# Kernel tuning notes

Hardware: AMD Instinct MI355X
Metric: run time of the kernel (lower is better)

## Reference

```python
import jax, jax.numpy as jnp
import numpy as np

DIM = 512
D_IN = 4096
N_OBJ = 2048
N_REL = 32768
STEPS = 2
N_OBJ_CLS = 151
N_REL_CLS = 51
EPS = 1e-5


def _mlp2(x, w1, b1, w2, b2):
    # Linear -> ReLU -> Linear (torch Linear: y = x W^T + b)
    return jnp.maximum(x @ w1.T + b1, 0.0) @ w2.T + b2


def _gate(a, b, w, bias):
    # Sequential(Linear(2*dim, 1), Sigmoid) on cat([a, b], 1)
    return jax.nn.sigmoid(jnp.concatenate([a, b], axis=1) @ w.T + bias)


def _gru_cell(x, h, wih, whh, bih, bhh):
    gi = x @ wih.T + bih  # [N, 3*DIM]
    gh = h @ whh.T + bhh
    ir, iz, inew = jnp.split(gi, 3, axis=1)
    hr, hz, hnew = jnp.split(gh, 3, axis=1)
    r = jax.nn.sigmoid(ir + hr)
    z = jax.nn.sigmoid(iz + hz)
    n = jnp.tanh(inew + r * hnew)
    return (1.0 - z) * n + z * h


def setup_inputs() -> dict:
    key = jax.random.key(0)
    ks = jax.random.split(key, 32)
    rn = lambda k, shape, s=0.02: jax.random.normal(k, shape, dtype=jnp.float32) * s
    z = lambda *shape: jnp.zeros(shape, dtype=jnp.float32)
    return {
        'x_obj': jax.random.normal(ks[0], (N_OBJ, D_IN), dtype=jnp.float32),
        'x_pred': jax.random.normal(ks[1], (N_REL, D_IN), dtype=jnp.float32),
        'rel_inds': jax.random.randint(ks[2], (N_REL, 2), 0, N_OBJ),
        # obj / pred embedding MLPs
        'oe_w1': rn(ks[3], (DIM, D_IN)), 'oe_b1': z(DIM),
        'oe_w2': rn(ks[4], (DIM, DIM)), 'oe_b2': z(DIM),
        'pe_w1': rn(ks[5], (DIM, D_IN)), 'pe_b1': z(DIM),
        'pe_w2': rn(ks[6], (DIM, DIM)), 'pe_b2': z(DIM),
        # gates: Linear(2*dim, 1)
        'g_sn_w': rn(ks[7], (1, 2 * DIM)), 'g_sn_b': z(1),
        'g_on_w': rn(ks[8], (1, 2 * DIM)), 'g_on_b': z(1),
        'g_se_w': rn(ks[9], (1, 2 * DIM)), 'g_se_b': z(1),
        'g_oe_w': rn(ks[10], (1, 2 * DIM)), 'g_oe_b': z(1),
        # GRU cells
        'ngru_wih': rn(ks[11], (3 * DIM, DIM)), 'ngru_whh': rn(ks[12], (3 * DIM, DIM)),
        'ngru_bih': z(3 * DIM), 'ngru_bhh': z(3 * DIM),
        'egru_wih': rn(ks[13], (3 * DIM, DIM)), 'egru_whh': rn(ks[14], (3 * DIM, DIM)),
        'egru_bih': z(3 * DIM), 'egru_bhh': z(3 * DIM),
        # classifier heads
        'op_w': rn(ks[15], (N_OBJ_CLS, DIM)), 'op_b': z(N_OBJ_CLS),
        'pp_w': rn(ks[16], (N_REL_CLS, DIM)), 'pp_b': z(N_REL_CLS),
    }


def reference(x_obj, x_pred, rel_inds,
              oe_w1, oe_b1, oe_w2, oe_b2,
              pe_w1, pe_b1, pe_w2, pe_b2,
              g_sn_w, g_sn_b, g_on_w, g_on_b,
              g_se_w, g_se_b, g_oe_w, g_oe_b,
              ngru_wih, ngru_whh, ngru_bih, ngru_bhh,
              egru_wih, egru_whh, egru_bih, egru_bhh,
              op_w, op_b, pp_w, pp_b):
    n_obj = x_obj.shape[0]
    subj_idx = rel_inds[:, 0]
    obj_idx = rel_inds[:, 1]

    h_obj = _mlp2(x_obj, oe_w1, oe_b1, oe_w2, oe_b2)    # [N_obj, DIM]
    h_edge = _mlp2(x_pred, pe_w1, pe_b1, pe_w2, pe_b2)  # [N_rel, DIM]

    # row sums of the 0/1 subj/obj_pred_map == in-degree counts (constants)
    ones = jnp.ones((rel_inds.shape[0],), dtype=jnp.float32)
    cnt_s = jax.ops.segment_sum(ones, subj_idx, num_segments=n_obj)[:, None]
    cnt_o = jax.ops.segment_sum(ones, obj_idx, num_segments=n_obj)[:, None]

    for _ in range(STEPS):
        sub_vert = h_obj[subj_idx]  # [N_rel, DIM]
        obj_vert = h_obj[obj_idx]

        # node update: gated edge->node messages, mean-aggregated per node
        msg_p2s = _gate(sub_vert, h_edge, g_sn_w, g_sn_b) * h_edge
        msg_p2o = _gate(obj_vert, h_edge, g_on_w, g_on_b) * h_edge
        node_message = (
            jax.ops.segment_sum(msg_p2s, subj_idx, num_segments=n_obj) / (cnt_s + EPS)
            + jax.ops.segment_sum(msg_p2o, obj_idx, num_segments=n_obj) / (cnt_o + EPS)
        ) / 2.0
        new_h_obj = _gru_cell(node_message, h_obj, ngru_wih, ngru_whh, ngru_bih, ngru_bhh)

        # edge update: gated node->edge messages
        msg_s2p = _gate(sub_vert, h_edge, g_se_w, g_se_b) * sub_vert
        msg_o2p = _gate(obj_vert, h_edge, g_oe_w, g_oe_b) * obj_vert
        edge_message = (msg_s2p + msg_o2p) / 2.0
        h_edge = _gru_cell(edge_message, h_edge, egru_wih, egru_whh, egru_bih, egru_bhh)
        h_obj = new_h_obj

    obj_class_logits = h_obj @ op_w.T + op_b    # [N_obj, 151]
    pred_class_logits = h_edge @ pp_w.T + pp_b  # [N_rel, 51]
    obj_class_labels = jnp.argmax(obj_class_logits[:, 1:], axis=1) + 1
    return (h_obj, h_edge, obj_class_logits, pred_class_logits, obj_class_labels, rel_inds)
```

## Files before the change

kernel.cpp:

```cpp
#include <hip/hip_runtime.h>
#include <math.h>

typedef unsigned short u16;
typedef unsigned int u32;
typedef _Float16 f16;
typedef f16 f16x8 __attribute__((ext_vector_type(8)));
typedef float f32x4 __attribute__((ext_vector_type(4)));

#define DIM 512
#define D_IN 4096
#define N_OBJS 2048
#define N_RELS 32768
#define N_OBJ_CLS 151
#define N_REL_CLS 51
#define EPSV 1e-5f

#define OFF_HOBJ  0
#define OFF_HEDGE (N_OBJS*DIM)
#define OFF_OLOG  (OFF_HEDGE + N_RELS*DIM)
#define OFF_PLOG  (OFF_OLOG + N_OBJS*N_OBJ_CLS)
#define OFF_LBL   (OFF_PLOG + N_RELS*N_REL_CLS)
#define OFF_RI    (OFF_LBL + N_OBJS)

__device__ __forceinline__ float sigmoidf_(float x) { return 1.0f / (1.0f + expf(-x)); }
__device__ __forceinline__ u16 f2h_(float f) {
    union { f16 h; u16 u; } c; c.h = (f16)f; return c.u;
}
__device__ __forceinline__ float h2f_(u16 u) {
    union { f16 h; u16 u; } c; c.u = u; return (float)c.h;
}

__device__ __forceinline__ void cvt8h1(const float* f, uint4& h) {
    u32 hh[8];
#pragma unroll
    for (int i = 0; i < 8; i++) hh[i] = f2h_(f[i]);
    h.x = hh[0] | (hh[1] << 16); h.y = hh[2] | (hh[3] << 16);
    h.z = hh[4] | (hh[5] << 16); h.w = hh[6] | (hh[7] << 16);
}
__device__ __forceinline__ void cvt8h2(const float* f, uint4& h, uint4& l) {
    u32 hh[8], ll[8];
#pragma unroll
    for (int i = 0; i < 8; i++) {
        u16 x = f2h_(f[i]);
        hh[i] = x;
        ll[i] = f2h_(f[i] - h2f_(x));
    }
    h.x = hh[0] | (hh[1] << 16); h.y = hh[2] | (hh[3] << 16);
    h.z = hh[4] | (hh[5] << 16); h.w = hh[6] | (hh[7] << 16);
    l.x = ll[0] | (ll[1] << 16); l.y = ll[2] | (ll[3] << 16);
    l.z = ll[4] | (ll[5] << 16); l.w = ll[6] | (ll[7] << 16);
}

__device__ __forceinline__ int swzo(int row, int c) {
    return row * 32 + ((c ^ ((row >> 1) & 3)) << 3);
}

__device__ __forceinline__ int xcdswz(int orig, int nwg) {
    const int q = nwg >> 3;
    return (orig & 7) * q + (orig >> 3);
}

__device__ __forceinline__ void gload16(const void* g, void* l) {
    __builtin_amdgcn_global_load_lds(
        (const __attribute__((address_space(1))) void*)g,
        (__attribute__((address_space(3))) void*)l, 16, 0, 0);
}

__global__ __launch_bounds__(256) void convert_h(const float* __restrict__ src,
    u16* __restrict__ hi, int n4)
{
    const int i = blockIdx.x * 256 + threadIdx.x;
    if (i >= n4) return;
    const float4 v = ((const float4*)src)[i];
    ((ushort4*)hi)[i] = make_ushort4(f2h_(v.x), f2h_(v.y), f2h_(v.z), f2h_(v.w));
}

template<bool RELU, int AT, bool WSPLIT>
__global__ __launch_bounds__(256, 3) void gemm_a32(
    const float* __restrict__ A, const u16* __restrict__ Bhi,
    const float* __restrict__ bias, u16* __restrict__ Chi, u16* __restrict__ Clo,
    int NX, int K)
{
    __shared__ u16 sAh[128 * 32], sBh[128 * 32];
    __shared__ u16 sAl[AT == 2 ? 128 * 32 : 1];
    const int id = xcdswz(blockIdx.x, gridDim.x);
    const int m0 = (id / NX) * 128, n0 = (id % NX) * 128;
    const int N = NX * 128;
    const int t = threadIdx.x;
    const int wid = t >> 6, lane = t & 63;
    const int wm = (wid >> 1) * 64, wn = (wid & 1) * 64;
    const int lr = lane & 15, lk = lane >> 4;

    f32x4 acc[4][4] = {};

    const int sr = t >> 1;
    const int sc = (t & 1) * 2;
    const float* Ap = A + (size_t)(m0 + sr) * K + (t & 1) * 16;

    const int rB = (wid * 2) * 16 + (lane >> 2);
    const int cB = (lane & 3) ^ ((rB >> 1) & 3);
    const u16* Bp0 = Bhi + (size_t)(n0 + rB) * K + cB * 8;
    const u16* Bp1 = Bp0 + (size_t)16 * K;
    u16* Bd0 = &sBh[(wid * 2) * 512];
    u16* Bd1 = Bd0 + 512;

    float fv[16];
    *(float4*)&fv[0]  = *(const float4*)(Ap);
    *(float4*)&fv[4]  = *(const float4*)(Ap + 4);
    *(float4*)&fv[8]  = *(const float4*)(Ap + 8);
    *(float4*)&fv[12] = *(const float4*)(Ap + 12);

    for (int k0 = 0; k0 < K; k0 += 32) {
        uint4 ah0, ah1, al0, al1;
        if (AT == 2) { cvt8h2(fv, ah0, al0); cvt8h2(fv + 8, ah1, al1); }
        else         { cvt8h1(fv, ah0);      cvt8h1(fv + 8, ah1); }

        __syncthreads();
        gload16(Bp0 + k0, Bd0);
        gload16(Bp1 + k0, Bd1);
        *(uint4*)&sAh[swzo(sr, sc)]     = ah0;
        *(uint4*)&sAh[swzo(sr, sc + 1)] = ah1;
        if (AT == 2) {
            *(uint4*)&sAl[swzo(sr, sc)]     = al0;
            *(uint4*)&sAl[swzo(sr, sc + 1)] = al1;
        }
        asm volatile("s_waitcnt vmcnt(0)" ::: "memory");
        __syncthreads();

        const int kn = k0 + 32;
        if (kn < K) {
            *(float4*)&fv[0]  = *(const float4*)(Ap + kn);
            *(float4*)&fv[4]  = *(const float4*)(Ap + kn + 4);
            *(float4*)&fv[8]  = *(const float4*)(Ap + kn + 8);
            *(float4*)&fv[12] = *(const float4*)(Ap + kn + 12);
        }

        f16x8 ah[4], al[4], bh[4];
#pragma unroll
        for (int f = 0; f < 4; f++) {
            const int off = swzo(wm + f * 16 + lr, lk);
            ah[f] = *(const f16x8*)&sAh[off];
            if (AT == 2) al[f] = *(const f16x8*)&sAl[off];
            bh[f] = *(const f16x8*)&sBh[swzo(wn + f * 16 + lr, lk)];
        }
#pragma unroll
        for (int fm = 0; fm < 4; fm++)
#pragma unroll
            for (int fn = 0; fn < 4; fn++) {
                acc[fm][fn] = __builtin_amdgcn_mfma_f32_16x16x32_f16(ah[fm], bh[fn], acc[fm][fn], 0, 0, 0);
                if (AT == 2)
                    acc[fm][fn] = __builtin_amdgcn_mfma_f32_16x16x32_f16(al[fm], bh[fn], acc[fm][fn], 0, 0, 0);
            }
    }
#pragma unroll
    for (int fm = 0; fm < 4; fm++) {
        const int mrow = m0 + wm + fm * 16 + lk * 4;
#pragma unroll
        for (int fn = 0; fn < 4; fn++) {
            const int col = n0 + wn + fn * 16 + lr;
            const float bv = bias[col];
#pragma unroll
            for (int j = 0; j < 4; j++) {
                float v = acc[fm][fn][j] + bv;
                if (RELU) v = fmaxf(v, 0.0f);
                const u16 h = f2h_(v);
                Chi[(size_t)(mrow + j) * N + col] = h;
                if (WSPLIT) Clo[(size_t)(mrow + j) * N + col] = f2h_(v - h2f_(h));
            }
        }
    }
}

template<int AT, bool WF32, bool WHI, bool WLO>
__global__ __launch_bounds__(256, AT == 1 ? 4 : 3) void gemm_f16(
    const u16* __restrict__ Ahi, const u16* __restrict__ Alo,
    const u16* __restrict__ Bhi, const float* __restrict__ bias,
    float* __restrict__ C32, u16* __restrict__ Chi, u16* __restrict__ Clo,
    int NX, int N, int ldc, int K)
{
    __shared__ u16 sAh[128 * 32], sBh[128 * 32];
    __shared__ u16 sAl[AT == 2 ? 128 * 32 : 1];
    const int id = xcdswz(blockIdx.x, gridDim.x);
    const int m0 = (id / NX) * 128, n0 = (id % NX) * 128;
    const int t = threadIdx.x;
    const int wid = t >> 6, lane = t & 63;
    const int wm = (wid >> 1) * 64, wn = (wid & 1) * 64;
    const int lr = lane & 15, lk = lane >> 4;

    f32x4 acc[4][4] = {};

    const int rr = (wid * 2) * 16 + (lane >> 2);
    const int cc = (lane & 3) ^ ((rr >> 1) & 3);
    const u16* pA0 = Ahi + (size_t)(m0 + rr) * K + cc * 8;
    const u16* pA1 = pA0 + (size_t)16 * K;
    const u16* pL0 = (AT == 2) ? Alo + (size_t)(m0 + rr) * K + cc * 8 : nullptr;
    const u16* pL1 = (AT == 2) ? pL0 + (size_t)16 * K : nullptr;
    const u16* pB0 = Bhi + (size_t)(n0 + rr) * K + cc * 8;
    const u16* pB1 = pB0 + (size_t)16 * K;
    u16* dA0 = &sAh[(wid * 2) * 512]; u16* dA1 = dA0 + 512;
    u16* dL0 = &sAl[(AT == 2) ? (wid * 2) * 512 : 0]; u16* dL1 = dL0 + ((AT == 2) ? 512 : 0);
    u16* dB0 = &sBh[(wid * 2) * 512]; u16* dB1 = dB0 + 512;

    for (int k0 = 0; k0 < K; k0 += 32) {
        __syncthreads();
        gload16(pA0 + k0, dA0); gload16(pA1 + k0, dA1);
        if (AT == 2) { gload16(pL0 + k0, dL0); gload16(pL1 + k0, dL1); }
        gload16(pB0 + k0, dB0); gload16(pB1 + k0, dB1);
        asm volatile("s_waitcnt vmcnt(0)" ::: "memory");
        __syncthreads();

        f16x8 ah[4], al[4], bh[4];
#pragma unroll
        for (int f = 0; f < 4; f++) {
            const int off = swzo(wm + f * 16 + lr, lk);
            ah[f] = *(const f16x8*)&sAh[off];
            if (AT == 2) al[f] = *(const f16x8*)&sAl[off];
            bh[f] = *(const f16x8*)&sBh[swzo(wn + f * 16 + lr, lk)];
        }
#pragma unroll
        for (int fm = 0; fm < 4; fm++)
#pragma unroll
            for (int fn = 0; fn < 4; fn++) {
                acc[fm][fn] = __builtin_amdgcn_mfma_f32_16x16x32_f16(ah[fm], bh[fn], acc[fm][fn], 0, 0, 0);
                if (AT == 2)
                    acc[fm][fn] = __builtin_amdgcn_mfma_f32_16x16x32_f16(al[fm], bh[fn], acc[fm][fn], 0, 0, 0);
            }
    }
#pragma unroll
    for (int fm = 0; fm < 4; fm++) {
        const int mrow = m0 + wm + fm * 16 + lk * 4;
#pragma unroll
        for (int fn = 0; fn < 4; fn++) {
            const int col = n0 + wn + fn * 16 + lr;
            const float bv = bias[col];
#pragma unroll
            for (int j = 0; j < 4; j++) {
                const float v = acc[fm][fn][j] + bv;
                if (WF32 && col < N) C32[(size_t)(mrow + j) * ldc + col] = v;
                if (WHI) {
                    const u16 h = f2h_(v);
                    Chi[(size_t)(mrow + j) * (NX * 128) + col] = h;
                    if (WLO)
                        Clo[(size_t)(mrow + j) * (NX * 128) + col] = f2h_(v - h2f_(h));
                }
            }
        }
    }
}

template<int AT>
__global__ __launch_bounds__(256, AT == 1 ? 4 : 3) void gru_gemm2(
    const u16* __restrict__ Xh, const u16* __restrict__ Xl,
    const u16* __restrict__ WiH, const float* __restrict__ bi, u16* __restrict__ gi,
    const u16* __restrict__ Hh, const u16* __restrict__ Hl,
    const u16* __restrict__ WhH, const float* __restrict__ bhs, u16* __restrict__ gh_,
    int K)
{
    __shared__ u16 sAh[128 * 32], sBh[128 * 32];
    __shared__ u16 sAl[AT == 2 ? 128 * 32 : 1];
    const int id = xcdswz(blockIdx.x, gridDim.x);
    const int part = id % 24;
    const int m0 = (id / 24) * 128;
    const bool isH = part >= 12;
    const u16* Ahi = isH ? Hh : Xh;
    const u16* Alo = isH ? Hl : Xl;
    const u16* Bhi = isH ? WhH : WiH;
    const float* bias = isH ? bhs : bi;
    u16* C = isH ? gh_ : gi;
    const int n0 = (part - (isH ? 12 : 0)) * 128;

    const int t = threadIdx.x;
    const int wid = t >> 6, lane = t & 63;
    const int wm = (wid >> 1) * 64, wn = (wid & 1) * 64;
    const int lr = lane & 15, lk = lane >> 4;

    f32x4 acc[4][4] = {};

    const int rr = (wid * 2) * 16 + (lane >> 2);
    const int cc = (lane & 3) ^ ((rr >> 1) & 3);
    const u16* pA0 = Ahi + (size_t)(m0 + rr) * K + cc * 8;
    const u16* pA1 = pA0 + (size_t)16 * K;
    const u16* pL0 = (AT == 2) ? Alo + (size_t)(m0 + rr) * K + cc * 8 : nullptr;
    const u16* pL1 = (AT == 2) ? pL0 + (size_t)16 * K : nullptr;
    const u16* pB0 = Bhi + (size_t)(n0 + rr) * K + cc * 8;
    const u16* pB1 = pB0 + (size_t)16 * K;
    u16* dA0 = &sAh[(wid * 2) * 512]; u16* dA1 = dA0 + 512;
    u16* dL0 = &sAl[(AT == 2) ? (wid * 2) * 512 : 0]; u16* dL1 = dL0 + ((AT == 2) ? 512 : 0);
    u16* dB0 = &sBh[(wid * 2) * 512]; u16* dB1 = dB0 + 512;

    for (int k0 = 0; k0 < K; k0 += 32) {
        __syncthreads();
        gload16(pA0 + k0, dA0); gload16(pA1 + k0, dA1);
        if (AT == 2) { gload16(pL0 + k0, dL0); gload16(pL1 + k0, dL1); }
        gload16(pB0 + k0, dB0); gload16(pB1 + k0, dB1);
        asm volatile("s_waitcnt vmcnt(0)" ::: "memory");
        __syncthreads();

        f16x8 ah[4], al[4], bh[4];
#pragma unroll
        for (int f = 0; f < 4; f++) {
            const int off = swzo(wm + f * 16 + lr, lk);
            ah[f] = *(const f16x8*)&sAh[off];
            if (AT == 2) al[f] = *(const f16x8*)&sAl[off];
            bh[f] = *(const f16x8*)&sBh[swzo(wn + f * 16 + lr, lk)];
        }
#pragma unroll
        for (int fm = 0; fm < 4; fm++)
#pragma unroll
            for (int fn = 0; fn < 4; fn++) {
                acc[fm][fn] = __builtin_amdgcn_mfma_f32_16x16x32_f16(ah[fm], bh[fn], acc[fm][fn], 0, 0, 0);
                if (AT == 2)
                    acc[fm][fn] = __builtin_amdgcn_mfma_f32_16x16x32_f16(al[fm], bh[fn], acc[fm][fn], 0, 0, 0);
            }
    }
#pragma unroll
    for (int fm = 0; fm < 4; fm++) {
        const int mrow = m0 + wm + fm * 16 + lk * 4;
#pragma unroll
        for (int fn = 0; fn < 4; fn++) {
            const int col = n0 + wn + fn * 16 + lr;
            const float bv = bias[col];
#pragma unroll
            for (int j = 0; j < 4; j++)
                C[(size_t)(mrow + j) * 1536 + col] = f2h_(acc[fm][fn][j] + bv);
        }
    }
}

__device__ __forceinline__ float gcomb(u16 ir, u16 iz, u16 in_, u16 hr, u16 hz,
                                       u16 hn, float h) {
    const float r = sigmoidf_(h2f_(ir) + h2f_(hr));
    const float z = sigmoidf_(h2f_(iz) + h2f_(hz));
    const float n = tanhf(h2f_(in_) + r * h2f_(hn));
    return (1.0f - z) * n + z * h;
}

template<bool WSPLIT, bool WF32>
__global__ __launch_bounds__(256) void gru_combine(
    const u16* __restrict__ gi, const u16* __restrict__ gh,
    u16* __restrict__ hh, u16* __restrict__ hl, float* __restrict__ H32, int R)
{
    const int idx = blockIdx.x * 256 + threadIdx.x;
    if (idx >= R * 128) return;
    const int r = idx >> 7, c4 = (idx & 127) * 4;
    const size_t gb = (size_t)r * 1536 + c4;
    const ushort4 ir4 = *(const ushort4*)&gi[gb];
    const ushort4 iz4 = *(const ushort4*)&gi[gb + 512];
    const ushort4 in4 = *(const ushort4*)&gi[gb + 1024];
    const ushort4 hr4 = *(const ushort4*)&gh[gb];
    const ushort4 hz4 = *(const ushort4*)&gh[gb + 512];
    const ushort4 hn4 = *(const ushort4*)&gh[gb + 1024];
    const size_t hb = (size_t)r * 512 + c4;
    const ushort4 hhi = *(const ushort4*)&hh[hb];
    float h0 = h2f_(hhi.x), h1 = h2f_(hhi.y), h2 = h2f_(hhi.z), h3 = h2f_(hhi.w);
    if (WSPLIT) {
        const ushort4 hlo = *(const ushort4*)&hl[hb];
        h0 += h2f_(hlo.x); h1 += h2f_(hlo.y); h2 += h2f_(hlo.z); h3 += h2f_(hlo.w);
    }
    float4 o;
    o.x = gcomb(ir4.x, iz4.x, in4.x, hr4.x, hz4.x, hn4.x, h0);
    o.y = gcomb(ir4.y, iz4.y, in4.y, hr4.y, hz4.y, hn4.y, h1);
    o.z = gcomb(ir4.z, iz4.z, in4.z, hr4.z, hz4.z, hn4.z, h2);
    o.w = gcomb(ir4.w, iz4.w, in4.w, hr4.w, hz4.w, hn4.w, h3);
    const ushort4 hi4 = make_ushort4(f2h_(o.x), f2h_(o.y), f2h_(o.z), f2h_(o.w));
    *(ushort4*)&hh[hb] = hi4;
    if (WSPLIT) {
        *(ushort4*)&hl[hb] = make_ushort4(
            f2h_(o.x - h2f_(hi4.x)), f2h_(o.y - h2f_(hi4.y)),
            f2h_(o.z - h2f_(hi4.z)), f2h_(o.w - h2f_(hi4.w)));
    }
    if (WF32) *(float4*)&H32[hb] = o;
}

__global__ __launch_bounds__(256) void count_int(const int* __restrict__ rel,
                                                 int* cs, int* co)
{
    const int e = blockIdx.x * 256 + threadIdx.x;
    atomicAdd(&cs[rel[2 * e]], 1);
    atomicAdd(&co[rel[2 * e + 1]], 1);
}

__global__ __launch_bounds__(256) void scan_off(const int* __restrict__ cs,
    const int* __restrict__ co, int* __restrict__ offs, int* __restrict__ offo)
{
    __shared__ int tmp[256];
    for (int arr = 0; arr < 2; arr++) {
        const int* c = arr ? co : cs;
        int* off = arr ? offo : offs;
        const int base = threadIdx.x * 8;
        int loc[8]; int s = 0;
#pragma unroll
        for (int j = 0; j < 8; j++) { loc[j] = c[base + j]; s += loc[j]; }
        tmp[threadIdx.x] = s;
        __syncthreads();
        for (int d = 1; d < 256; d <<= 1) {
            const int v = (threadIdx.x >= d) ? tmp[threadIdx.x - d] : 0;
            __syncthreads();
            tmp[threadIdx.x] += v;
            __syncthreads();
        }
        int p = tmp[threadIdx.x] - s;
#pragma unroll
        for (int j = 0; j < 8; j++) { off[base + j] = p; p += loc[j]; }
        __syncthreads();
    }
}

__global__ __launch_bounds__(256) void fill_csr(const int* __restrict__ rel,
    int* curS, int* curO, const int* __restrict__ offs, const int* __restrict__ offo,
    int* __restrict__ listS, int* __restrict__ listO)
{
    const int e = blockIdx.x * 256 + threadIdx.x;
    const int s = rel[2 * e], o = rel[2 * e + 1];
    const int i = atomicAdd(&curS[s], 1);
    listS[offs[s] + i] = e;
    const int j = atomicAdd(&curO[o], 1);
    listO[offo[o] + j] = e;
}

__global__ __launch_bounds__(256) void gatepass(
    const u16* __restrict__ hho, const u16* __restrict__ hhe,
    const int* __restrict__ rel,
    const float* __restrict__ wsn, const float* __restrict__ bsn,
    const float* __restrict__ won, const float* __restrict__ bon,
    const float* __restrict__ wse, const float* __restrict__ bse,
    const float* __restrict__ woe, const float* __restrict__ boe,
    const int* __restrict__ cs, const int* __restrict__ co,
    u16* __restrict__ emh, float* __restrict__ af, float* __restrict__ ag)
{
    __shared__ float red[4][4];
    const int e = blockIdx.x;
    const int t = threadIdx.x;
    const int wid = t >> 6, lane = t & 63;
    const int s = rel[2 * e], o = rel[2 * e + 1];
    const int c = 2 * t;

    const u32 hsu = *(const u32*)&hho[(size_t)s * DIM + c];
    const u32 hou = *(const u32*)&hho[(size_t)o * DIM + c];
    const u32 heu = *(const u32*)&hhe[(size_t)e * DIM + c];
    const float hsx = h2f_((u16)hsu), hsy = h2f_((u16)(hsu >> 16));
    const float hox = h2f_((u16)hou), hoy = h2f_((u16)(hou >> 16));
    const float hex = h2f_((u16)heu), hey = h2f_((u16)(heu >> 16));

    const float2 w0v = *(const float2*)&wsn[c], w0e = *(const float2*)&wsn[DIM + c];
    const float2 w1v = *(const float2*)&won[c], w1e = *(const float2*)&won[DIM + c];
    const float2 w2v = *(const float2*)&wse[c], w2e = *(const float2*)&wse[DIM + c];
    const float2 w3v = *(const float2*)&woe[c], w3e = *(const float2*)&woe[DIM + c];

    float p0 = hsx * w0v.x + hsy * w0v.y + hex * w0e.x + hey * w0e.y;
    float p1 = hox * w1v.x + hoy * w1v.y + hex * w1e.x + hey * w1e.y;
    float p2 = hsx * w2v.x + hsy * w2v.y + hex * w2e.x + hey * w2e.y;
    float p3 = hox * w3v.x + hoy * w3v.y + hex * w3e.x + hey * w3e.y;

#pragma unroll
    for (int off = 32; off; off >>= 1) {
        p0 += __shfl_xor(p0, off);
        p1 += __shfl_xor(p1, off);
        p2 += __shfl_xor(p2, off);
        p3 += __shfl_xor(p3, off);
    }
    if (lane == 0) { red[wid][0] = p0; red[wid][1] = p1; red[wid][2] = p2; red[wid][3] = p3; }
    __syncthreads();
    const float gsn = sigmoidf_(red[0][0] + red[1][0] + red[2][0] + red[3][0] + bsn[0]);
    const float gon = sigmoidf_(red[0][1] + red[1][1] + red[2][1] + red[3][1] + bon[0]);
    const float gse = sigmoidf_(red[0][2] + red[1][2] + red[2][2] + red[3][2] + bse[0]);
    const float goe = sigmoidf_(red[0][3] + red[1][3] + red[2][3] + red[3][3] + boe[0]);

    if (t == 0) {
        af[e] = 0.5f * gsn / ((float)cs[s] + EPSV);
        ag[e] = 0.5f * gon / ((float)co[o] + EPSV);
    }
    const float ex = 0.5f * (gse * hsx + goe * hox);
    const float ey = 0.5f * (gse * hsy + goe * hoy);
    *(u32*)&emh[(size_t)e * DIM + c] = (u32)f2h_(ex) | ((u32)f2h_(ey) << 16);
}

__global__ __launch_bounds__(256) void gather_nm(
    const u16* __restrict__ hhe,
    const int* __restrict__ listS, const int* __restrict__ listO,
    const int* __restrict__ offs, const int* __restrict__ offo,
    const int* __restrict__ cs, const int* __restrict__ co,
    const float* __restrict__ af, const float* __restrict__ ag,
    u16* __restrict__ nmh, u16* __restrict__ nml)
{
    const int v = blockIdx.x * 4 + (threadIdx.x >> 6);
    const int lane = threadIdx.x & 63;
    const int c = lane * 8;

    float acc[8] = {};
#pragma unroll
    for (int side = 0; side < 2; side++) {
        const int* list = side ? listO : listS;
        const int b = side ? offo[v] : offs[v];
        const int n = side ? co[v] : cs[v];
        const float* coef = side ? ag : af;
        for (int i = 0; i < n; i++) {
            const int e = list[b + i];
            const float a = coef[e];
            const uint4 x = *(const uint4*)&hhe[(size_t)e * DIM + c];
            acc[0] += a * h2f_((u16)x.x); acc[1] += a * h2f_((u16)(x.x >> 16));
            acc[2] += a * h2f_((u16)x.y); acc[3] += a * h2f_((u16)(x.y >> 16));
            acc[4] += a * h2f_((u16)x.z); acc[5] += a * h2f_((u16)(x.z >> 16));
            acc[6] += a * h2f_((u16)x.w); acc[7] += a * h2f_((u16)(x.w >> 16));
        }
    }
    u16 hi8[8], lo8[8];
#pragma unroll
    for (int j = 0; j < 8; j++) {
        hi8[j] = f2h_(acc[j]);
        lo8[j] = f2h_(acc[j] - h2f_(hi8[j]));
    }
    *(uint4*)&nmh[(size_t)v * DIM + c] = *(const uint4*)hi8;
    *(uint4*)&nml[(size_t)v * DIM + c] = *(const uint4*)lo8;
}

__global__ __launch_bounds__(256) void argmax_kernel(const float* __restrict__ logits,
                                                     float* __restrict__ out)
{
    const int row = blockIdx.x * 4 + (threadIdx.x >> 6);
    const int lane = threadIdx.x & 63;
    float bv = -1e30f; int bi = 1;
    for (int j = 1 + lane; j < N_OBJ_CLS; j += 64) {
        const float v = logits[(size_t)row * N_OBJ_CLS + j];
        if (v > bv) { bv = v; bi = j; }
    }
#pragma unroll
    for (int off = 32; off; off >>= 1) {
        const float ov = __shfl_xor(bv, off);
        const int oi = __shfl_xor(bi, off);
        if (ov > bv || (ov == bv && oi < bi)) { bv = ov; bi = oi; }
    }
    if (lane == 0) out[row] = (float)bi;
}

__global__ __launch_bounds__(256) void relinds_kernel(const int* __restrict__ rel,
                                                      float* __restrict__ out)
{
    const int i = blockIdx.x * 256 + threadIdx.x;
    out[i] = (float)rel[i];
}

extern "C" void kernel_launch(void* const* d_in, const int* in_sizes, int n_in,
                              void* d_out, int out_size, void* d_ws, size_t ws_size,
                              hipStream_t stream)
{
    const float* x_obj = (const float*)d_in[0];
    const float* x_pred = (const float*)d_in[1];
    const int* rel = (const int*)d_in[2];
    const float* oe_w1 = (const float*)d_in[3];
    const float* oe_b1 = (const float*)d_in[4];
    const float* oe_w2 = (const float*)d_in[5];
    const float* oe_b2 = (const float*)d_in[6];
    const float* pe_w1 = (const float*)d_in[7];
    const float* pe_b1 = (const float*)d_in[8];
    const float* pe_w2 = (const float*)d_in[9];
    const float* pe_b2 = (const float*)d_in[10];
    const float* g_sn_w = (const float*)d_in[11];
    const float* g_sn_b = (const float*)d_in[12];
    const float* g_on_w = (const float*)d_in[13];
    const float* g_on_b = (const float*)d_in[14];
    const float* g_se_w = (const float*)d_in[15];
    const float* g_se_b = (const float*)d_in[16];
    const float* g_oe_w = (const float*)d_in[17];
    const float* g_oe_b = (const float*)d_in[18];
    const float* ngru_wih = (const float*)d_in[19];
    const float* ngru_whh = (const float*)d_in[20];
    const float* ngru_bih = (const float*)d_in[21];
    const float* ngru_bhh = (const float*)d_in[22];
    const float* egru_wih = (const float*)d_in[23];
    const float* egru_whh = (const float*)d_in[24];
    const float* egru_bih = (const float*)d_in[25];
    const float* egru_bhh = (const float*)d_in[26];
    const float* op_w = (const float*)d_in[27];
    const float* op_b = (const float*)d_in[28];
    const float* pp_w = (const float*)d_in[29];
    const float* pp_b = (const float*)d_in[30];

    float* out = (float*)d_out;

    float* h_obj = out + OFF_HOBJ;
    float* h_edge = out + OFF_HEDGE;

    char* wsp = (char*)d_ws;
    float* af = (float*)wsp; wsp += N_RELS * 4;
    float* ag = (float*)wsp; wsp += N_RELS * 4;
    int* cs = (int*)wsp;   wsp += N_OBJS * 4;
    int* co = (int*)wsp;   wsp += N_OBJS * 4;
    int* offs = (int*)wsp; wsp += N_OBJS * 4;
    int* offo = (int*)wsp; wsp += N_OBJS * 4;
    int* curS = (int*)wsp; wsp += N_OBJS * 4;
    int* curO = (int*)wsp; wsp += N_OBJS * 4;
    int* listS = (int*)wsp; wsp += N_RELS * 4;
    int* listO = (int*)wsp; wsp += N_RELS * 4;

    u16* wp = (u16*)wsp;
    const int s_big = DIM * D_IN, s_sq = DIM * DIM, s_gru = 3 * DIM * DIM;
    u16 *oe1h = wp; wp += s_big;
    u16 *pe1h = wp; wp += s_big;
    u16 *oe2h = wp; wp += s_sq;
    u16 *pe2h = wp; wp += s_sq;
    u16 *nih_h = wp; wp += s_gru;
    u16 *nhh_h = wp; wp += s_gru;
    u16 *eih_h = wp; wp += s_gru;
    u16 *ehh_h = wp; wp += s_gru;
    u16 *oph = wp; wp += 256 * DIM;
    u16 *pph = wp; wp += 128 * DIM;
    u16 *tmpo_h = wp; wp += (size_t)N_OBJS * DIM;
    u16 *tmpo_l = wp; wp += (size_t)N_OBJS * DIM;
    u16 *tmpe_h = wp; wp += (size_t)N_RELS * DIM;
    u16 *hhoh = wp; wp += (size_t)N_OBJS * DIM;
    u16 *hhol = wp; wp += (size_t)N_OBJS * DIM;
    u16 *hhe  = wp; wp += (size_t)N_RELS * DIM;
    u16 *emh  = wp; wp += (size_t)N_RELS * DIM;
    u16 *nmh  = wp; wp += (size_t)N_OBJS * DIM;
    u16 *nml  = wp; wp += (size_t)N_OBJS * DIM;

    const size_t used = (size_t)((char*)wp - (char*)d_ws);
    int R = 8192;
    if (used + (size_t)32768 * 6144 <= ws_size) R = 32768;
    else if (used + (size_t)16384 * 6144 <= ws_size) R = 16384;
    u16* gi = wp;
    u16* gh = gi + (size_t)R * 1536;

    auto cvtw = [&](const float* s, u16* h, int n) {
        convert_h<<<(n / 4 + 255) / 256, 256, 0, stream>>>(s, h, n / 4);
    };
    cvtw(oe_w1, oe1h, s_big);
    cvtw(pe_w1, pe1h, s_big);
    cvtw(oe_w2, oe2h, s_sq);
    cvtw(pe_w2, pe2h, s_sq);
    cvtw(ngru_wih, nih_h, s_gru);
    cvtw(ngru_whh, nhh_h, s_gru);
    cvtw(egru_wih, eih_h, s_gru);
    cvtw(egru_whh, ehh_h, s_gru);
    cvtw(op_w, oph, N_OBJ_CLS * DIM);
    cvtw(pp_w, pph, N_REL_CLS * DIM);

    hipMemsetAsync(cs, 0, 2 * N_OBJS * sizeof(int), stream);
    hipMemsetAsync(curS, 0, 2 * N_OBJS * sizeof(int), stream);
    count_int<<<N_RELS / 256, 256, 0, stream>>>(rel, cs, co);
    scan_off<<<1, 256, 0, stream>>>(cs, co, offs, offo);
    fill_csr<<<N_RELS / 256, 256, 0, stream>>>(rel, curS, curO, offs, offo, listS, listO);

    gemm_a32<true, 2, true><<<4 * (N_OBJS / 128), 256, 0, stream>>>(
        x_obj, oe1h, oe_b1, tmpo_h, tmpo_l, 4, D_IN);
    gemm_f16<2, false, true, true><<<4 * (N_OBJS / 128), 256, 0, stream>>>(
        tmpo_h, tmpo_l, oe2h, oe_b2, nullptr, hhoh, hhol, 4, DIM, DIM, DIM);
    gemm_a32<true, 1, false><<<4 * (N_RELS / 128), 256, 0, stream>>>(
        x_pred, pe1h, pe_b1, tmpe_h, nullptr, 4, D_IN);
    gemm_f16<1, false, true, false><<<4 * (N_RELS / 128), 256, 0, stream>>>(
        tmpe_h, nullptr, pe2h, pe_b2, nullptr, hhe, nullptr, 4, DIM, DIM, DIM);

    for (int step = 0; step < 2; step++) {
        gatepass<<<N_RELS, 256, 0, stream>>>(
            hhoh, hhe, rel,
            g_sn_w, g_sn_b, g_on_w, g_on_b, g_se_w, g_se_b, g_oe_w, g_oe_b,
            cs, co, emh, af, ag);
        gather_nm<<<N_OBJS / 4, 256, 0, stream>>>(
            hhe, listS, listO, offs, offo, cs, co, af, ag, nmh, nml);

        gru_gemm2<2><<<24 * (N_OBJS / 128), 256, 0, stream>>>(
            nmh, nml, nih_h, ngru_bih, gi, hhoh, hhol, nhh_h, ngru_bhh, gh, DIM);
        if (step == 0)
            gru_combine<true, false><<<(N_OBJS * 128 + 255) / 256, 256, 0, stream>>>(
                gi, gh, hhoh, hhol, nullptr, N_OBJS);
        else
            gru_combine<true, true><<<(N_OBJS * 128 + 255) / 256, 256, 0, stream>>>(
                gi, gh, hhoh, hhol, h_obj, N_OBJS);

        for (int r0 = 0; r0 < N_RELS; r0 += R) {
            const int Rc = (N_RELS - r0 < R) ? (N_RELS - r0) : R;
            gru_gemm2<1><<<24 * (Rc / 128), 256, 0, stream>>>(
                emh + (size_t)r0 * DIM, nullptr, eih_h, egru_bih, gi,
                hhe + (size_t)r0 * DIM, nullptr, ehh_h, egru_bhh, gh, DIM);
            if (step == 0)
                gru_combine<false, false><<<(Rc * 128 + 255) / 256, 256, 0, stream>>>(
                    gi, gh, hhe + (size_t)r0 * DIM, nullptr, nullptr, Rc);
            else
                gru_combine<false, true><<<(Rc * 128 + 255) / 256, 256, 0, stream>>>(
                    gi, gh, hhe + (size_t)r0 * DIM, nullptr, h_edge + (size_t)r0 * DIM, Rc);
        }
    }

    gemm_f16<2, true, false, false><<<2 * (N_OBJS / 128), 256, 0, stream>>>(
        hhoh, hhol, oph, op_b, out + OFF_OLOG, nullptr, nullptr,
        2, N_OBJ_CLS, N_OBJ_CLS, DIM);
    gemm_f16<1, true, false, false><<<1 * (N_RELS / 128), 256, 0, stream>>>(
        hhe, nullptr, pph, pp_b, out + OFF_PLOG, nullptr, nullptr,
        1, N_REL_CLS, N_REL_CLS, DIM);

    argmax_kernel<<<N_OBJS / 4, 256, 0, stream>>>(out + OFF_OLOG, out + OFF_LBL);
    relinds_kernel<<<(2 * N_RELS) / 256, 256, 0, stream>>>(rel, out + OFF_RI);
}
```

Before: 1.102 ms.

## Double-buffer LDS tiles in GEMM kernels to overlap global loads with MFMA

Turns the single shared-memory tiles in gemm_a32, gemm_f16 and gru_gemm2 into ping-pong buffers. The loads for the next K-slice are issued before the MFMAs on the current slice, which removes one barrier per iteration and the explicit vmcnt(0) wait. The aim is to hide global-to-LDS latency behind compute. In exchange, LDS use per block doubles, which can limit occupancy. The explicit wait on the async LDS loads is also gone, so correctness depends on __syncthreads waiting for them to finish.

```diff
diff --git a/kernel.cpp b/kernel.cpp
--- a/kernel.cpp
+++ b/kernel.cpp
@@ -81,8 +81,8 @@
     const float* __restrict__ bias, u16* __restrict__ Chi, u16* __restrict__ Clo,
     int NX, int K)
 {
-    __shared__ u16 sAh[128 * 32], sBh[128 * 32];
-    __shared__ u16 sAl[AT == 2 ? 128 * 32 : 1];
+    __shared__ u16 sAh[2][128 * 32], sBh[2][128 * 32];
+    __shared__ u16 sAl[AT == 2 ? 2 : 1][AT == 2 ? 128 * 32 : 1];
     const int id = xcdswz(blockIdx.x, gridDim.x);
     const int m0 = (id / NX) * 128, n0 = (id % NX) * 128;
     const int N = NX * 128;
@@ -101,34 +101,33 @@
     const int cB = (lane & 3) ^ ((rB >> 1) & 3);
     const u16* Bp0 = Bhi + (size_t)(n0 + rB) * K + cB * 8;
     const u16* Bp1 = Bp0 + (size_t)16 * K;
-    u16* Bd0 = &sBh[(wid * 2) * 512];
-    u16* Bd1 = Bd0 + 512;
+    const int bOff = (wid * 2) * 512;
 
     float fv[16];
     *(float4*)&fv[0]  = *(const float4*)(Ap);
     *(float4*)&fv[4]  = *(const float4*)(Ap + 4);
     *(float4*)&fv[8]  = *(const float4*)(Ap + 8);
     *(float4*)&fv[12] = *(const float4*)(Ap + 12);
-
+    gload16(Bp0, &sBh[0][bOff]);
+    gload16(Bp1, &sBh[0][bOff + 512]);
+
+    int cur = 0;
     for (int k0 = 0; k0 < K; k0 += 32) {
         uint4 ah0, ah1, al0, al1;
         if (AT == 2) { cvt8h2(fv, ah0, al0); cvt8h2(fv + 8, ah1, al1); }
         else         { cvt8h1(fv, ah0);      cvt8h1(fv + 8, ah1); }
-
-        __syncthreads();
-        gload16(Bp0 + k0, Bd0);
-        gload16(Bp1 + k0, Bd1);
-        *(uint4*)&sAh[swzo(sr, sc)]     = ah0;
-        *(uint4*)&sAh[swzo(sr, sc + 1)] = ah1;
+        *(uint4*)&sAh[cur][swzo(sr, sc)]     = ah0;
+        *(uint4*)&sAh[cur][swzo(sr, sc + 1)] = ah1;
         if (AT == 2) {
-            *(uint4*)&sAl[swzo(sr, sc)]     = al0;
-            *(uint4*)&sAl[swzo(sr, sc + 1)] = al1;
-        }
-        asm volatile("s_waitcnt vmcnt(0)" ::: "memory");
+            *(uint4*)&sAl[cur][swzo(sr, sc)]     = al0;
+            *(uint4*)&sAl[cur][swzo(sr, sc + 1)] = al1;
+        }
         __syncthreads();
 
         const int kn = k0 + 32;
         if (kn < K) {
+            gload16(Bp0 + kn, &sBh[cur ^ 1][bOff]);
+            gload16(Bp1 + kn, &sBh[cur ^ 1][bOff + 512]);
             *(float4*)&fv[0]  = *(const float4*)(Ap + kn);
             *(float4*)&fv[4]  = *(const float4*)(Ap + kn + 4);
             *(float4*)&fv[8]  = *(const float4*)(Ap + kn + 8);
@@ -139,9 +138,9 @@
 #pragma unroll
         for (int f = 0; f < 4; f++) {
             const int off = swzo(wm + f * 16 + lr, lk);
-            ah[f] = *(const f16x8*)&sAh[off];
-            if (AT == 2) al[f] = *(const f16x8*)&sAl[off];
-            bh[f] = *(const f16x8*)&sBh[swzo(wn + f * 16 + lr, lk)];
+            ah[f] = *(const f16x8*)&sAh[cur][off];
+            if (AT == 2) al[f] = *(const f16x8*)&sAl[cur][off];
+            bh[f] = *(const f16x8*)&sBh[cur][swzo(wn + f * 16 + lr, lk)];
         }
 #pragma unroll
         for (int fm = 0; fm < 4; fm++)
@@ -151,6 +150,7 @@
                 if (AT == 2)
                     acc[fm][fn] = __builtin_amdgcn_mfma_f32_16x16x32_f16(al[fm], bh[fn], acc[fm][fn], 0, 0, 0);
             }
+        cur ^= 1;
     }
 #pragma unroll
     for (int fm = 0; fm < 4; fm++) {
@@ -178,8 +178,8 @@
     float* __restrict__ C32, u16* __restrict__ Chi, u16* __restrict__ Clo,
     int NX, int N, int ldc, int K)
 {
-    __shared__ u16 sAh[128 * 32], sBh[128 * 32];
-    __shared__ u16 sAl[AT == 2 ? 128 * 32 : 1];
+    __shared__ u16 sAh[2][128 * 32], sBh[2][128 * 32];
+    __shared__ u16 sAl[AT == 2 ? 2 : 1][AT == 2 ? 128 * 32 : 1];
     const int id = xcdswz(blockIdx.x, gridDim.x);
     const int m0 = (id / NX) * 128, n0 = (id % NX) * 128;
     const int t = threadIdx.x;
@@ -197,25 +197,34 @@
     const u16* pL1 = (AT == 2) ? pL0 + (size_t)16 * K : nullptr;
     const u16* pB0 = Bhi + (size_t)(n0 + rr) * K + cc * 8;
     const u16* pB1 = pB0 + (size_t)16 * K;
-    u16* dA0 = &sAh[(wid * 2) * 512]; u16* dA1 = dA0 + 512;
-    u16* dL0 = &sAl[(AT == 2) ? (wid * 2) * 512 : 0]; u16* dL1 = dL0 + ((AT == 2) ? 512 : 0);
-    u16* dB0 = &sBh[(wid * 2) * 512]; u16* dB1 = dB0 + 512;
-
+    const int bOff = (wid * 2) * 512;
+
+    gload16(pA0, &sAh[0][bOff]); gload16(pA1, &sAh[0][bOff + 512]);
+    if (AT == 2) { gload16(pL0, &sAl[0][bOff]); gload16(pL1, &sAl[0][bOff + 512]); }
+    gload16(pB0, &sBh[0][bOff]); gload16(pB1, &sBh[0][bOff + 512]);
+
+    int cur = 0;
     for (int k0 = 0; k0 < K; k0 += 32) {
         __syncthreads();
-        gload16(pA0 + k0, dA0); gload16(pA1 + k0, dA1);
-        if (AT == 2) { gload16(pL0 + k0, dL0); gload16(pL1 + k0, dL1); }
-        gload16(pB0 + k0, dB0); gload16(pB1 + k0, dB1);
-        asm volatile("s_waitcnt vmcnt(0)" ::: "memory");
-        __syncthreads();
+        const int kn = k0 + 32;
+        if (kn < K) {
+            gload16(pA0 + kn, &sAh[cur ^ 1][bOff]);
+            gload16(pA1 + kn, &sAh[cur ^ 1][bOff + 512]);
+            if (AT == 2) {
+                gload16(pL0 + kn, &sAl[cur ^ 1][bOff]);
+                gload16(pL1 + kn, &sAl[cur ^ 1][bOff + 512]);
+            }
+            gload16(pB0 + kn, &sBh[cur ^ 1][bOff]);
+            gload16(pB1 + kn, &sBh[cur ^ 1][bOff + 512]);
+        }
 
         f16x8 ah[4], al[4], bh[4];
 #pragma unroll
         for (int f = 0; f < 4; f++) {
             const int off = swzo(wm + f * 16 + lr, lk);
-            ah[f] = *(const f16x8*)&sAh[off];
-            if (AT == 2) al[f] = *(const f16x8*)&sAl[off];
-            bh[f] = *(const f16x8*)&sBh[swzo(wn + f * 16 + lr, lk)];
+            ah[f] = *(const f16x8*)&sAh[cur][off];
+            if (AT == 2) al[f] = *(const f16x8*)&sAl[cur][off];
+            bh[f] = *(const f16x8*)&sBh[cur][swzo(wn + f * 16 + lr, lk)];
         }
 #pragma unroll
         for (int fm = 0; fm < 4; fm++)
@@ -225,6 +234,7 @@
                 if (AT == 2)
                     acc[fm][fn] = __builtin_amdgcn_mfma_f32_16x16x32_f16(al[fm], bh[fn], acc[fm][fn], 0, 0, 0);
             }
+        cur ^= 1;
     }
 #pragma unroll
     for (int fm = 0; fm < 4; fm++) {
@@ -256,8 +266,8 @@
     const u16* __restrict__ WhH, const float* __restrict__ bhs, u16* __restrict__ gh_,
     int K)
 {
-    __shared__ u16 sAh[128 * 32], sBh[128 * 32];
-    __shared__ u16 sAl[AT == 2 ? 128 * 32 : 1];
+    __shared__ u16 sAh[2][128 * 32], sBh[2][128 * 32];
+    __shared__ u16 sAl[AT == 2 ? 2 : 1][AT == 2 ? 128 * 32 : 1];
     const int id = xcdswz(blockIdx.x, gridDim.x);
     const int part = id % 24;
     const int m0 = (id / 24) * 128;
@@ -284,25 +294,34 @@
     const u16* pL1 = (AT == 2) ? pL0 + (size_t)16 * K : nullptr;
     const u16* pB0 = Bhi + (size_t)(n0 + rr) * K + cc * 8;
     const u16* pB1 = pB0 + (size_t)16 * K;
-    u16* dA0 = &sAh[(wid * 2) * 512]; u16* dA1 = dA0 + 512;
-    u16* dL0 = &sAl[(AT == 2) ? (wid * 2) * 512 : 0]; u16* dL1 = dL0 + ((AT == 2) ? 512 : 0);
-    u16* dB0 = &sBh[(wid * 2) * 512]; u16* dB1 = dB0 + 512;
-
+    const int bOff = (wid * 2) * 512;
+
+    gload16(pA0, &sAh[0][bOff]); gload16(pA1, &sAh[0][bOff + 512]);
+    if (AT == 2) { gload16(pL0, &sAl[0][bOff]); gload16(pL1, &sAl[0][bOff + 512]); }
+    gload16(pB0, &sBh[0][bOff]); gload16(pB1, &sBh[0][bOff + 512]);
+
+    int cur = 0;
     for (int k0 = 0; k0 < K; k0 += 32) {
         __syncthreads();
-        gload16(pA0 + k0, dA0); gload16(pA1 + k0, dA1);
-        if (AT == 2) { gload16(pL0 + k0, dL0); gload16(pL1 + k0, dL1); }
-        gload16(pB0 + k0, dB0); gload16(pB1 + k0, dB1);
-        asm volatile("s_waitcnt vmcnt(0)" ::: "memory");
-        __syncthreads();
+        const int kn = k0 + 32;
+        if (kn < K) {
+            gload16(pA0 + kn, &sAh[cur ^ 1][bOff]);
+            gload16(pA1 + kn, &sAh[cur ^ 1][bOff + 512]);
+            if (AT == 2) {
+                gload16(pL0 + kn, &sAl[cur ^ 1][bOff]);
+                gload16(pL1 + kn, &sAl[cur ^ 1][bOff + 512]);
+            }
+            gload16(pB0 + kn, &sBh[cur ^ 1][bOff]);
+            gload16(pB1 + kn, &sBh[cur ^ 1][bOff + 512]);
+        }
 
         f16x8 ah[4], al[4], bh[4];
 #pragma unroll
         for (int f = 0; f < 4; f++) {
             const int off = swzo(wm + f * 16 + lr, lk);
-            ah[f] = *(const f16x8*)&sAh[off];
-            if (AT == 2) al[f] = *(const f16x8*)&sAl[off];
-            bh[f] = *(const f16x8*)&sBh[swzo(wn + f * 16 + lr, lk)];
+            ah[f] = *(const f16x8*)&sAh[cur][off];
+            if (AT == 2) al[f] = *(const f16x8*)&sAl[cur][off];
+            bh[f] = *(const f16x8*)&sBh[cur][swzo(wn + f * 16 + lr, lk)];
         }
 #pragma unroll
         for (int fm = 0; fm < 4; fm++)
@@ -312,6 +331,7 @@
                 if (AT == 2)
                     acc[fm][fn] = __builtin_amdgcn_mfma_f32_16x16x32_f16(al[fm], bh[fn], acc[fm][fn], 0, 0, 0);
             }
+        cur ^= 1;
     }
 #pragma unroll
     for (int fm = 0; fm < 4; fm++) {
```

New measurement: 1.181 ms. +7.1%, slower.

## Double-buffer A prefetch in fp32 GEMM and use one wave per edge in gatepass

Applied to the files above, without the earlier changes.

The fp32-input GEMM now keeps two register buffers for A and prefetches two K-steps ahead, so each global load has more time to land before it is converted and used. The gate kernel is restructured to process one edge per 64-lane wave with 16-byte loads. This removes the shared-memory reduction and the block barrier, and launches a quarter as many blocks. The cost is higher register pressure in the GEMM, and the unrolled step now assumes K is a multiple of 64.

```diff
diff --git a/kernel.cpp b/kernel.cpp
--- a/kernel.cpp
+++ b/kernel.cpp
@@ -104,20 +104,24 @@
     u16* Bd0 = &sBh[(wid * 2) * 512];
     u16* Bd1 = Bd0 + 512;
 
-    float fv[16];
-    *(float4*)&fv[0]  = *(const float4*)(Ap);
-    *(float4*)&fv[4]  = *(const float4*)(Ap + 4);
-    *(float4*)&fv[8]  = *(const float4*)(Ap + 8);
-    *(float4*)&fv[12] = *(const float4*)(Ap + 12);
-
-    for (int k0 = 0; k0 < K; k0 += 32) {
+    float fvA[16], fvB[16];
+    *(float4*)&fvA[0]  = *(const float4*)(Ap);
+    *(float4*)&fvA[4]  = *(const float4*)(Ap + 4);
+    *(float4*)&fvA[8]  = *(const float4*)(Ap + 8);
+    *(float4*)&fvA[12] = *(const float4*)(Ap + 12);
+    *(float4*)&fvB[0]  = *(const float4*)(Ap + 32);
+    *(float4*)&fvB[4]  = *(const float4*)(Ap + 32 + 4);
+    *(float4*)&fvB[8]  = *(const float4*)(Ap + 32 + 8);
+    *(float4*)&fvB[12] = *(const float4*)(Ap + 32 + 12);
+
+    auto step = [&](int kk, float (&fv)[16], int kpre) {
         uint4 ah0, ah1, al0, al1;
         if (AT == 2) { cvt8h2(fv, ah0, al0); cvt8h2(fv + 8, ah1, al1); }
         else         { cvt8h1(fv, ah0);      cvt8h1(fv + 8, ah1); }
 
         __syncthreads();
-        gload16(Bp0 + k0, Bd0);
-        gload16(Bp1 + k0, Bd1);
+        gload16(Bp0 + kk, Bd0);
+        gload16(Bp1 + kk, Bd1);
         *(uint4*)&sAh[swzo(sr, sc)]     = ah0;
         *(uint4*)&sAh[swzo(sr, sc + 1)] = ah1;
         if (AT == 2) {
@@ -127,12 +131,11 @@
         asm volatile("s_waitcnt vmcnt(0)" ::: "memory");
         __syncthreads();
 
-        const int kn = k0 + 32;
-        if (kn < K) {
-            *(float4*)&fv[0]  = *(const float4*)(Ap + kn);
-            *(float4*)&fv[4]  = *(const float4*)(Ap + kn + 4);
-            *(float4*)&fv[8]  = *(const float4*)(Ap + kn + 8);
-            *(float4*)&fv[12] = *(const float4*)(Ap + kn + 12);
+        if (kpre < K) {
+            *(float4*)&fv[0]  = *(const float4*)(Ap + kpre);
+            *(float4*)&fv[4]  = *(const float4*)(Ap + kpre + 4);
+            *(float4*)&fv[8]  = *(const float4*)(Ap + kpre + 8);
+            *(float4*)&fv[12] = *(const float4*)(Ap + kpre + 12);
         }
 
         f16x8 ah[4], al[4], bh[4];
@@ -151,6 +154,11 @@
                 if (AT == 2)
                     acc[fm][fn] = __builtin_amdgcn_mfma_f32_16x16x32_f16(al[fm], bh[fn], acc[fm][fn], 0, 0, 0);
             }
+    };
+
+    for (int k0 = 0; k0 < K; k0 += 64) {
+        step(k0, fvA, k0 + 64);
+        step(k0 + 32, fvB, k0 + 96);
     }
 #pragma unroll
     for (int fm = 0; fm < 4; fm++) {
@@ -428,30 +436,51 @@
     const int* __restrict__ cs, const int* __restrict__ co,
     u16* __restrict__ emh, float* __restrict__ af, float* __restrict__ ag)
 {
-    __shared__ float red[4][4];
-    const int e = blockIdx.x;
-    const int t = threadIdx.x;
-    const int wid = t >> 6, lane = t & 63;
+    const int e = blockIdx.x * 4 + (threadIdx.x >> 6);
+    const int lane = threadIdx.x & 63;
     const int s = rel[2 * e], o = rel[2 * e + 1];
-    const int c = 2 * t;
-
-    const u32 hsu = *(const u32*)&hho[(size_t)s * DIM + c];
-    const u32 hou = *(const u32*)&hho[(size_t)o * DIM + c];
-    const u32 heu = *(const u32*)&hhe[(size_t)e * DIM + c];
-    const float hsx = h2f_((u16)hsu), hsy = h2f_((u16)(hsu >> 16));
-    const float hox = h2f_((u16)hou), hoy = h2f_((u16)(hou >> 16));
-    const float hex = h2f_((u16)heu), hey = h2f_((u16)(heu >> 16));
-
-    const float2 w0v = *(const float2*)&wsn[c], w0e = *(const float2*)&wsn[DIM + c];
-    const float2 w1v = *(const float2*)&won[c], w1e = *(const float2*)&won[DIM + c];
-    const float2 w2v = *(const float2*)&wse[c], w2e = *(const float2*)&wse[DIM + c];
-    const float2 w3v = *(const float2*)&woe[c], w3e = *(const float2*)&woe[DIM + c];
-
-    float p0 = hsx * w0v.x + hsy * w0v.y + hex * w0e.x + hey * w0e.y;
-    float p1 = hox * w1v.x + hoy * w1v.y + hex * w1e.x + hey * w1e.y;
-    float p2 = hsx * w2v.x + hsy * w2v.y + hex * w2e.x + hey * w2e.y;
-    float p3 = hox * w3v.x + hoy * w3v.y + hex * w3e.x + hey * w3e.y;
-
+    const int c = lane * 8;
+
+    const uint4 hsu = *(const uint4*)&hho[(size_t)s * DIM + c];
+    const uint4 hou = *(const uint4*)&hho[(size_t)o * DIM + c];
+    const uint4 heu = *(const uint4*)&hhe[(size_t)e * DIM + c];
+    float hs[8], ho[8], he[8];
+    hs[0] = h2f_((u16)hsu.x); hs[1] = h2f_((u16)(hsu.x >> 16));
+    hs[2] = h2f_((u16)hsu.y); hs[3] = h2f_((u16)(hsu.y >> 16));
+    hs[4] = h2f_((u16)hsu.z); hs[5] = h2f_((u16)(hsu.z >> 16));
+    hs[6] = h2f_((u16)hsu.w); hs[7] = h2f_((u16)(hsu.w >> 16));
+    ho[0] = h2f_((u16)hou.x); ho[1] = h2f_((u16)(hou.x >> 16));
+    ho[2] = h2f_((u16)hou.y); ho[3] = h2f_((u16)(hou.y >> 16));
+    ho[4] = h2f_((u16)hou.z); ho[5] = h2f_((u16)(hou.z >> 16));
+    ho[6] = h2f_((u16)hou.w); ho[7] = h2f_((u16)(hou.w >> 16));
+    he[0] = h2f_((u16)heu.x); he[1] = h2f_((u16)(heu.x >> 16));
+    he[2] = h2f_((u16)heu.y); he[3] = h2f_((u16)(heu.y >> 16));
+    he[4] = h2f_((u16)heu.z); he[5] = h2f_((u16)(heu.z >> 16));
+    he[6] = h2f_((u16)heu.w); he[7] = h2f_((u16)(heu.w >> 16));
+
+    float p0 = 0.f, p1 = 0.f, p2 = 0.f, p3 = 0.f;
+#pragma unroll
+    for (int q = 0; q < 2; q++) {
+        const float4 w0v = *(const float4*)&wsn[c + q * 4];
+        const float4 w0e = *(const float4*)&wsn[DIM + c + q * 4];
+        const float4 w1v = *(const float4*)&won[c + q * 4];
+        const float4 w1e = *(const float4*)&won[DIM + c + q * 4];
+        const float4 w2v = *(const float4*)&wse[c + q * 4];
+        const float4 w2e = *(const float4*)&wse[DIM + c + q * 4];
+        const float4 w3v = *(const float4*)&woe[c + q * 4];
+        const float4 w3e = *(const float4*)&woe[DIM + c + q * 4];
+        const float* s4 = &hs[q * 4];
+        const float* o4 = &ho[q * 4];
+        const float* e4 = &he[q * 4];
+        p0 += s4[0]*w0v.x + s4[1]*w0v.y + s4[2]*w0v.z + s4[3]*w0v.w
+            + e4[0]*w0e.x + e4[1]*w0e.y + e4[2]*w0e.z + e4[3]*w0e.w;
+        p1 += o4[0]*w1v.x + o4[1]*w1v.y + o4[2]*w1v.z + o4[3]*w1v.w
+            + e4[0]*w1e.x + e4[1]*w1e.y + e4[2]*w1e.z + e4[3]*w1e.w;
+        p2 += s4[0]*w2v.x + s4[1]*w2v.y + s4[2]*w2v.z + s4[3]*w2v.w
+            + e4[0]*w2e.x + e4[1]*w2e.y + e4[2]*w2e.z + e4[3]*w2e.w;
+        p3 += o4[0]*w3v.x + o4[1]*w3v.y + o4[2]*w3v.z + o4[3]*w3v.w
+            + e4[0]*w3e.x + e4[1]*w3e.y + e4[2]*w3e.z + e4[3]*w3e.w;
+    }
 #pragma unroll
     for (int off = 32; off; off >>= 1) {
         p0 += __shfl_xor(p0, off);
@@ -459,20 +488,20 @@
         p2 += __shfl_xor(p2, off);
         p3 += __shfl_xor(p3, off);
     }
-    if (lane == 0) { red[wid][0] = p0; red[wid][1] = p1; red[wid][2] = p2; red[wid][3] = p3; }
-    __syncthreads();
-    const float gsn = sigmoidf_(red[0][0] + red[1][0] + red[2][0] + red[3][0] + bsn[0]);
-    const float gon = sigmoidf_(red[0][1] + red[1][1] + red[2][1] + red[3][1] + bon[0]);
-    const float gse = sigmoidf_(red[0][2] + red[1][2] + red[2][2] + red[3][2] + bse[0]);
-    const float goe = sigmoidf_(red[0][3] + red[1][3] + red[2][3] + red[3][3] + boe[0]);
-
-    if (t == 0) {
+    const float gsn = sigmoidf_(p0 + bsn[0]);
+    const float gon = sigmoidf_(p1 + bon[0]);
+    const float gse = sigmoidf_(p2 + bse[0]);
+    const float goe = sigmoidf_(p3 + boe[0]);
+
+    if (lane == 0) {
         af[e] = 0.5f * gsn / ((float)cs[s] + EPSV);
         ag[e] = 0.5f * gon / ((float)co[o] + EPSV);
     }
-    const float ex = 0.5f * (gse * hsx + goe * hox);
-    const float ey = 0.5f * (gse * hsy + goe * hoy);
-    *(u32*)&emh[(size_t)e * DIM + c] = (u32)f2h_(ex) | ((u32)f2h_(ey) << 16);
+    u16 em8[8];
+#pragma unroll
+    for (int j = 0; j < 8; j++)
+        em8[j] = f2h_(0.5f * (gse * hs[j] + goe * ho[j]));
+    *(uint4*)&emh[(size_t)e * DIM + c] = *(const uint4*)em8;
 }
 
 __global__ __launch_bounds__(256) void gather_nm(
@@ -652,7 +681,7 @@
         tmpe_h, nullptr, pe2h, pe_b2, nullptr, hhe, nullptr, 4, DIM, DIM, DIM);
 
     for (int step = 0; step < 2; step++) {
-        gatepass<<<N_RELS, 256, 0, stream>>>(
+        gatepass<<<N_RELS / 4, 256, 0, stream>>>(
             hhoh, hhe, rel,
             g_sn_w, g_sn_b, g_on_w, g_on_b, g_se_w, g_se_b, g_oe_w, g_oe_b,
             cs, co, emh, af, ag);
```

Result: no change. 1.107 ms (+0.4%).
